# Kernel optimization log

Hardware: AMD Instinct MI355X
Metric: run time of the kernel (lower is better)

## Reference

```python
import jax, jax.numpy as jnp
import numpy as np

N_HEADS = 8
HEAD_C = 48
NC = N_HEADS * HEAD_C  # 384
N_GROUPS = 4
GC = NC // N_GROUPS  # 96
STRIDE = 2
EPS = 1e-5


def conv1x1(x, w, b):
    # x: (B,C,H,W), w: (O,C), b: (O,)
    return jnp.einsum('bchw,oc->bohw', x, w) + b[None, :, None, None]


def ref_points(Hk, Wk, dtype):
    ry = jnp.linspace(0.5, Hk - 0.5, Hk, dtype=dtype) / (Hk - 1.0) * 2.0 - 1.0
    rx = jnp.linspace(0.5, Wk - 0.5, Wk, dtype=dtype) / (Wk - 1.0) * 2.0 - 1.0
    return jnp.stack(jnp.meshgrid(ry, rx, indexing='ij'), axis=-1)  # (Hk,Wk,2) in (y,x)


def grid_sample_bilinear(img, grid):
    # img: (N,C,H,W); grid: (N,Hg,Wg,2) xy in [-1,1]; align_corners=True, zeros padding
    N, C, H, W = img.shape
    gx = (grid[..., 0] + 1.0) * 0.5 * (W - 1)
    gy = (grid[..., 1] + 1.0) * 0.5 * (H - 1)
    x0 = jnp.floor(gx); y0 = jnp.floor(gy)
    x1 = x0 + 1.0;      y1 = y0 + 1.0
    wx1 = gx - x0; wx0 = 1.0 - wx1
    wy1 = gy - y0; wy0 = 1.0 - wy1

    def gather(ix, iy):
        valid = (ix >= 0) & (ix <= W - 1) & (iy >= 0) & (iy <= H - 1)
        ixc = jnp.clip(ix, 0, W - 1).astype(jnp.int32)
        iyc = jnp.clip(iy, 0, H - 1).astype(jnp.int32)
        vals = jax.vmap(lambda im, yy, xx: im[:, yy, xx])(img, iyc, ixc)  # (N,C,Hg,Wg)
        return vals * valid[:, None].astype(img.dtype)

    v00 = gather(x0, y0); v01 = gather(x1, y0)
    v10 = gather(x0, y1); v11 = gather(x1, y1)
    return (v00 * (wx0 * wy0)[:, None] + v01 * (wx1 * wy0)[:, None]
            + v10 * (wx0 * wy1)[:, None] + v11 * (wx1 * wy1)[:, None])


def _forward(x, Wq, bq, Wk, bk, Wv, bv, Wo, bo,
             off_dw_w, off_dw_b, ln_g, ln_b, off_pw_w):
    B, C, H, W = x.shape
    q = conv1x1(x, Wq, bq)                               # (B,C,H,W)
    q_off = q.reshape(B * N_GROUPS, GC, H, W)
    # offset net: depthwise 3x3 stride-2 conv -> channel LN -> GELU -> 1x1 to 2 ch
    h = jax.lax.conv_general_dilated(
        q_off, off_dw_w, (STRIDE, STRIDE), ((1, 1), (1, 1)),
        dimension_numbers=('NCHW', 'OIHW', 'NCHW'), feature_group_count=GC)
    h = h + off_dw_b[None, :, None, None]
    mu = h.mean(axis=1, keepdims=True)
    var = ((h - mu) ** 2).mean(axis=1, keepdims=True)
    h = (h - mu) / jnp.sqrt(var + EPS) * ln_g[None, :, None, None] + ln_b[None, :, None, None]
    h = jax.nn.gelu(h, approximate=False)
    offset = jnp.einsum('bchw,oc->bohw', h, off_pw_w)    # (B*g, 2, Hk, Wk), ch0=y, ch1=x
    Hk, Wk_ = offset.shape[2], offset.shape[3]
    rng = jnp.array([1.0 / (Hk - 1.0), 1.0 / (Wk_ - 1.0)], x.dtype).reshape(1, 2, 1, 1)
    offset = jnp.tanh(offset) * rng                      # offset_range_factor = 1
    offset = offset.transpose(0, 2, 3, 1)                # (B*g, Hk, Wk, 2) yx
    ref = ref_points(Hk, Wk_, x.dtype)                   # (Hk, Wk, 2) yx
    pos = offset + ref[None]
    xs = grid_sample_bilinear(x.reshape(B * N_GROUPS, GC, H, W), pos[..., ::-1])
    n = Hk * Wk_
    xs = xs.reshape(B, C, 1, n)
    k = conv1x1(xs, Wk, bk).reshape(B * N_HEADS, HEAD_C, n)
    v = conv1x1(xs, Wv, bv).reshape(B * N_HEADS, HEAD_C, n)
    qh = q.reshape(B * N_HEADS, HEAD_C, H * W)
    attn = jnp.einsum('bcm,bcn->bmn', qh, k) * (HEAD_C ** -0.5)
    attn = jax.nn.softmax(attn, axis=2)
    out = jnp.einsum('bmn,bcn->bcm', attn, v).reshape(B, C, H, W)
    y = conv1x1(out, Wo, bo)
    ref_b = jnp.broadcast_to(ref[None, None], (B, N_GROUPS, Hk, Wk_, 2))
    return y, pos.reshape(B, N_GROUPS, Hk, Wk_, 2), ref_b


def setup_inputs() -> dict:
    key = jax.random.key(0)
    ks = jax.random.split(key, 12)
    s = 0.02
    return {
        'x': jax.random.normal(ks[0], (8, NC, 56, 56), jnp.float32),
        'Wq': jax.random.normal(ks[1], (NC, NC), jnp.float32) * s,
        'bq': jnp.zeros((NC,), jnp.float32),
        'Wk': jax.random.normal(ks[2], (NC, NC), jnp.float32) * s,
        'bk': jnp.zeros((NC,), jnp.float32),
        'Wv': jax.random.normal(ks[3], (NC, NC), jnp.float32) * s,
        'bv': jnp.zeros((NC,), jnp.float32),
        'Wo': jax.random.normal(ks[4], (NC, NC), jnp.float32) * s,
        'bo': jnp.zeros((NC,), jnp.float32),
        'off_dw_w': jax.random.normal(ks[5], (GC, 1, 3, 3), jnp.float32) * 0.1,
        'off_dw_b': jnp.zeros((GC,), jnp.float32),
        'ln_g': jnp.ones((GC,), jnp.float32),
        'ln_b': jnp.zeros((GC,), jnp.float32),
        'off_pw_w': jax.random.normal(ks[6], (2, GC), jnp.float32) * 0.1,
    }


def reference(x, Wq, bq, Wk, bk, Wv, bv, Wo, bo,
              off_dw_w, off_dw_b, ln_g, ln_b, off_pw_w):
    return _forward(x, Wq, bq, Wk, bk, Wv, bv, Wo, bo,
                    off_dw_w, off_dw_b, ln_g, ln_b, off_pw_w)
```

## Files before the change

### kernel.cpp

```cpp
#include <hip/hip_runtime.h>
#include <math.h>

constexpr int BATCH = 8;
constexpr int NC    = 384;
constexpr int H     = 56, W = 56, HW = 3136;
constexpr int NPTS  = 784;
constexpr int NG    = 4, GC = 96;
constexpr int NH    = 8, HC = 48;

typedef __attribute__((ext_vector_type(8))) short short8;
typedef __attribute__((ext_vector_type(4))) float f32x4;
typedef __attribute__((ext_vector_type(4))) unsigned short us4;

__device__ inline unsigned short f2bf(float f) {
    union { float f; unsigned u; } v; v.f = f;
    unsigned r = v.u + 0x7FFF + ((v.u >> 16) & 1);
    return (unsigned short)(r >> 16);
}
__device__ inline float bf2f(unsigned short u) {
    union { unsigned u; float f; } v; v.u = (unsigned)u << 16;
    return v.f;
}
__device__ inline float wred_sum(float v) {
    #pragma unroll
    for (int off = 32; off > 0; off >>= 1) v += __shfl_xor(v, off);
    return v;
}

__global__ __launch_bounds__(256) void transpose_cvt(
    const float* __restrict__ x, unsigned short* __restrict__ xT)
{
    __shared__ unsigned short Ls[64 * 68];
    int b = blockIdx.z, c0 = blockIdx.y * 64, hw0 = blockIdx.x * 64;
    const float* xb = x + ((size_t)b * NC + c0) * HW + hw0;
    int t = threadIdx.x;
    #pragma unroll
    for (int i = 0; i < 4; i++) {
        int u = t + i * 256;
        int cc = u >> 4, f4 = (u & 15) * 4;
        float4 v = *(const float4*)&xb[(size_t)cc * HW + f4];
        us4 p; p[0] = f2bf(v.x); p[1] = f2bf(v.y); p[2] = f2bf(v.z); p[3] = f2bf(v.w);
        *(us4*)&Ls[cc * 68 + f4] = p;
    }
    __syncthreads();
    unsigned short* xTb = xT + ((size_t)b * HW + hw0) * NC + c0;
    #pragma unroll
    for (int i = 0; i < 4; i++) {
        int u = t + i * 256;
        int hw = u >> 4, cg = (u & 15) * 4;
        us4 p;
        p[0] = Ls[(cg + 0) * 68 + hw];
        p[1] = Ls[(cg + 1) * 68 + hw];
        p[2] = Ls[(cg + 2) * 68 + hw];
        p[3] = Ls[(cg + 3) * 68 + hw];
        *(us4*)&xTb[(size_t)hw * NC + cg] = p;
    }
}

__global__ __launch_bounds__(256) void wcvt(
    const float* __restrict__ w0, const float* __restrict__ w1,
    const float* __restrict__ w2, const float* __restrict__ w3,
    unsigned short* __restrict__ o0, unsigned short* __restrict__ okv,
    unsigned short* __restrict__ o3)
{
    const float* src; unsigned short* dst;
    switch (blockIdx.y) {
        case 0: src = w0; dst = o0; break;
        case 1: src = w1; dst = okv; break;
        case 2: src = w2; dst = okv + NC * NC; break;
        default: src = w3; dst = o3; break;
    }
    int idx = (blockIdx.x * 256 + threadIdx.x) * 4;
    float4 v = *(const float4*)&src[idx];
    us4 p; p[0] = f2bf(v.x); p[1] = f2bf(v.y); p[2] = f2bf(v.z); p[3] = f2bf(v.w);
    *(us4*)&dst[idx] = p;
}

template<int MODE>
__global__ __launch_bounds__(256) void gemm_bf16(
    const unsigned short* __restrict__ A, const float* __restrict__ bias,
    const float* __restrict__ bias2, const unsigned short* __restrict__ BT,
    float* __restrict__ Cf, unsigned short* __restrict__ Cb,
    unsigned short* __restrict__ Cb2, int N)
{
    int b  = blockIdx.z;
    int n0 = blockIdx.x * 128;
    int m0 = blockIdx.y * 128;
    const unsigned short* BTb = BT + (size_t)b * N * NC;

    __shared__ unsigned short As[128 * 40];
    __shared__ unsigned short Bs[128 * 40];

    int t = threadIdx.x;
    int wave = t >> 6, lane = t & 63;
    int quad = lane >> 4, col = lane & 15;
    int wm = (wave >> 1) * 64, wn = (wave & 1) * 64;

    const short8 z8 = {0,0,0,0,0,0,0,0};
    f32x4 acc[4][4];
    #pragma unroll
    for (int i = 0; i < 4; i++)
        #pragma unroll
        for (int j = 0; j < 4; j++) acc[i][j] = (f32x4){0.f, 0.f, 0.f, 0.f};

    for (int k0 = 0; k0 < NC; k0 += 32) {
        #pragma unroll
        for (int i = 0; i < 2; i++) {
            int u = t + i * 256;
            int mm = u >> 2, kc = (u & 3) * 8;
            *(short8*)&As[mm * 40 + kc] =
                *(const short8*)&A[(size_t)(m0 + mm) * NC + k0 + kc];
        }
        #pragma unroll
        for (int i = 0; i < 2; i++) {
            int u = t + i * 256;
            int nn = u >> 2, kc = (u & 3) * 8;
            short8 val = z8;
            if (n0 + nn < N)
                val = *(const short8*)&BTb[(size_t)(n0 + nn) * NC + k0 + kc];
            *(short8*)&Bs[nn * 40 + kc] = val;
        }
        __syncthreads();

        short8 af[4], bf[4];
        #pragma unroll
        for (int mt = 0; mt < 4; mt++)
            af[mt] = *(const short8*)&As[(wm + mt * 16 + col) * 40 + quad * 8];
        #pragma unroll
        for (int nt = 0; nt < 4; nt++)
            bf[nt] = *(const short8*)&Bs[(wn + nt * 16 + col) * 40 + quad * 8];
        #pragma unroll
        for (int mt = 0; mt < 4; mt++)
            #pragma unroll
            for (int nt = 0; nt < 4; nt++)
                acc[mt][nt] = __builtin_amdgcn_mfma_f32_16x16x32_bf16(
                    af[mt], bf[nt], acc[mt][nt], 0, 0, 0);
        __syncthreads();
    }

    if constexpr (MODE == 0) {
        float* Cfb = Cf + (size_t)b * NC * N;
        #pragma unroll
        for (int mt = 0; mt < 4; mt++) {
            #pragma unroll
            for (int r = 0; r < 4; r++) {
                int m = m0 + wm + mt * 16 + quad * 4 + r;
                float bv = bias[m];
                #pragma unroll
                for (int nt = 0; nt < 4; nt++) {
                    int n = n0 + wn + nt * 16 + col;
                    if (n < N) Cfb[(size_t)m * N + n] = acc[mt][nt][r] + bv;
                }
            }
        }
    } else if constexpr (MODE == 2) {
        unsigned short* Kb = Cb + (size_t)b * N * NC;
        #pragma unroll
        for (int mt = 0; mt < 4; mt++) {
            int mb = m0 + wm + mt * 16 + quad * 4;
            float bv[4];
            #pragma unroll
            for (int r = 0; r < 4; r++) bv[r] = bias[mb + r];
            #pragma unroll
            for (int nt = 0; nt < 4; nt++) {
                int n = n0 + wn + nt * 16 + col;
                if (n < N) {
                    us4 p;
                    #pragma unroll
                    for (int r = 0; r < 4; r++) p[r] = f2bf(acc[mt][nt][r] + bv[r]);
                    *(us4*)&Kb[(size_t)n * NC + mb] = p;
                }
            }
        }
    } else {
        if (m0 < NC) {
            unsigned short* Kb = Cb + (size_t)b * N * NC;
            #pragma unroll
            for (int mt = 0; mt < 4; mt++) {
                int mb = m0 + wm + mt * 16 + quad * 4;
                float bv[4];
                #pragma unroll
                for (int r = 0; r < 4; r++) bv[r] = bias[mb + r];
                #pragma unroll
                for (int nt = 0; nt < 4; nt++) {
                    int n = n0 + wn + nt * 16 + col;
                    if (n < N) {
                        us4 p;
                        #pragma unroll
                        for (int r = 0; r < 4; r++) p[r] = f2bf(acc[mt][nt][r] + bv[r]);
                        *(us4*)&Kb[(size_t)n * NC + mb] = p;
                    }
                }
            }
        } else {
            unsigned short* Vb = Cb2 + (size_t)b * NC * N;
            #pragma unroll
            for (int mt = 0; mt < 4; mt++) {
                #pragma unroll
                for (int r = 0; r < 4; r++) {
                    int m = m0 - NC + wm + mt * 16 + quad * 4 + r;
                    float bv = bias2[m];
                    #pragma unroll
                    for (int nt = 0; nt < 4; nt++) {
                        int n = n0 + wn + nt * 16 + col;
                        if (n < N) Vb[(size_t)m * N + n] = f2bf(acc[mt][nt][r] + bv);
                    }
                }
            }
        }
    }
}

__global__ __launch_bounds__(256) void offset_kernel(
    const unsigned short* __restrict__ qT, const float* __restrict__ dww,
    const float* __restrict__ dwb, const float* __restrict__ lng,
    const float* __restrict__ lnb, const float* __restrict__ pww,
    float* __restrict__ pos_out,   float* __restrict__ ref_out)
{
    int wave = threadIdx.x >> 6, l = threadIdx.x & 63;
    int bg = blockIdx.y, b = bg >> 2, g = bg & 3;
    int s  = blockIdx.x * 4 + wave;
    int py = s / 28, px = s - py * 28;
    bool has2 = l < 32;
    int c0 = l, c1 = 64 + l;

    const unsigned short* qb = qT + (size_t)b * HW * NC + g * GC;

    float h0 = 0.f, h1 = 0.f;
    #pragma unroll
    for (int ky = 0; ky < 3; ky++) {
        int yy = py * 2 - 1 + ky;
        if (yy < 0 || yy >= H) continue;
        #pragma unroll
        for (int kx = 0; kx < 3; kx++) {
            int xx = px * 2 - 1 + kx;
            if (xx < 0 || xx >= W) continue;
            const unsigned short* row = qb + (size_t)(yy * W + xx) * NC;
            float w0 = dww[c0 * 9 + ky * 3 + kx];
            h0 = fmaf(bf2f(row[c0]), w0, h0);
            if (has2) {
                float w1 = dww[c1 * 9 + ky * 3 + kx];
                h1 = fmaf(bf2f(row[c1]), w1, h1);
            }
        }
    }
    h0 += dwb[c0];
    if (has2) h1 += dwb[c1];

    float mu = wred_sum(h0 + (has2 ? h1 : 0.f)) * (1.f / GC);
    float d0 = h0 - mu, d1 = h1 - mu;
    float var = wred_sum(d0 * d0 + (has2 ? d1 * d1 : 0.f)) * (1.f / GC);
    float rstd = rsqrtf(var + 1e-5f);

    float hn0 = d0 * rstd * lng[c0] + lnb[c0];
    float ge0 = 0.5f * hn0 * (1.f + erff(hn0 * 0.70710678118654752f));
    float ge1 = 0.f;
    if (has2) {
        float hn1 = d1 * rstd * lng[c1] + lnb[c1];
        ge1 = 0.5f * hn1 * (1.f + erff(hn1 * 0.70710678118654752f));
    }

    float offy = wred_sum(ge0 * pww[c0] + (has2 ? ge1 * pww[c1] : 0.f));
    float offx = wred_sum(ge0 * pww[GC + c0] + (has2 ? ge1 * pww[GC + c1] : 0.f));

    if (l == 0) {
        float ry = (2.f * py + 1.f) / 27.f - 1.f;
        float rx = (2.f * px + 1.f) / 27.f - 1.f;
        size_t idx = ((size_t)bg * NPTS + s) * 2;
        pos_out[idx]     = tanhf(offy) * (1.f / 27.f) + ry;
        pos_out[idx + 1] = tanhf(offx) * (1.f / 27.f) + rx;
        ref_out[idx]     = ry;
        ref_out[idx + 1] = rx;
    }
}

__global__ __launch_bounds__(256) void sample_kernel(
    const unsigned short* __restrict__ xT, const float* __restrict__ pos,
    unsigned short* __restrict__ xsT)
{
    int bg = blockIdx.y;
    int b  = bg >> 2, g = bg & 3;
    int s  = blockIdx.x * 8 + (threadIdx.x >> 5);
    int l  = threadIdx.x & 31;

    const float* pg = pos + ((size_t)bg * NPTS + s) * 2;
    float py = pg[0], px = pg[1];
    float gx = (px + 1.f) * 27.5f;
    float gy = (py + 1.f) * 27.5f;
    float x0f = floorf(gx), y0f = floorf(gy);
    int ix0 = (int)x0f, iy0 = (int)y0f;
    int ix1 = ix0 + 1,  iy1 = iy0 + 1;
    float wx1 = gx - x0f, wx0 = 1.f - wx1;
    float wy1 = gy - y0f, wy0 = 1.f - wy1;
    bool vx0 = (ix0 >= 0) && (ix0 < W);
    bool vx1 = (ix1 >= 0) && (ix1 < W);
    bool vy0 = (iy0 >= 0) && (iy0 < H);
    bool vy1 = (iy1 >= 0) && (iy1 < H);
    int cx0 = vx0 ? ix0 : 0, cx1 = vx1 ? ix1 : 0;
    int cy0 = vy0 ? iy0 : 0, cy1 = vy1 ? iy1 : 0;
    float w00 = (vx0 && vy0) ? wx0 * wy0 : 0.f;
    float w01 = (vx1 && vy0) ? wx1 * wy0 : 0.f;
    float w10 = (vx0 && vy1) ? wx0 * wy1 : 0.f;
    float w11 = (vx1 && vy1) ? wx1 * wy1 : 0.f;

    const unsigned short* xb = xT + (size_t)b * HW * NC + g * GC;
    const unsigned short* r00 = xb + (size_t)(cy0 * W + cx0) * NC;
    const unsigned short* r01 = xb + (size_t)(cy0 * W + cx1) * NC;
    const unsigned short* r10 = xb + (size_t)(cy1 * W + cx0) * NC;
    const unsigned short* r11 = xb + (size_t)(cy1 * W + cx1) * NC;
    unsigned short* orow = xsT + ((size_t)b * NPTS + s) * NC + g * GC;
    #pragma unroll
    for (int ci = 0; ci < 3; ci++) {
        int c = l + ci * 32;
        float val = bf2f(r00[c]) * w00 + bf2f(r01[c]) * w01
                  + bf2f(r10[c]) * w10 + bf2f(r11[c]) * w11;
        orow[c] = f2bf(val);
    }
}

#define KS_STRIDE 56
#define VS_STRIDE 136

__device__ inline short8 scale8(short8 v, float s) {
    short8 r;
    #pragma unroll
    for (int j = 0; j < 8; j++) {
        unsigned short b = (unsigned short)v[j];
        r[j] = (short)f2bf(bf2f(b) * s);
    }
    return r;
}

union pun8 { short8 s8; unsigned u[4]; };

__global__ __launch_bounds__(256) void attn_mfma(
    const unsigned short* __restrict__ qT, const unsigned short* __restrict__ kt,
    const unsigned short* __restrict__ vt, unsigned short* __restrict__ aoT)
{
    __shared__ __align__(16) unsigned short smem[128 * KS_STRIDE + 48 * VS_STRIDE];
    unsigned short* Ks = smem;
    unsigned short* Vs = Ks + 128 * KS_STRIDE;

    int t    = threadIdx.x;
    int wave = t >> 6, lane = t & 63;
    int quad = lane >> 4, col = lane & 15;

    int bh = blockIdx.y;
    int b  = bh >> 3, h = bh & 7;
    int m0 = blockIdx.x * 128;
    const unsigned short* KT = kt + (size_t)b * NPTS * NC + h * HC;
    const unsigned short* VT = vt + ((size_t)b * NC + h * HC) * NPTS;

    const float scale = 0.14433756729740643f * 1.4426950408889634f;
    const short8 z8 = {0,0,0,0,0,0,0,0};

    short ones_v = (col == 0) ? (short)0x3F80 : (short)0;
    short8 ones8 = {ones_v, ones_v, ones_v, ones_v, ones_v, ones_v, ones_v, ones_v};

    int gmq[2];
    short8 qb0[2], qb1[2];
    #pragma unroll
    for (int set = 0; set < 2; set++) {
        int gm = m0 + wave * 32 + set * 16 + col;
        gmq[set] = gm;
        int cg = gm < HW ? gm : HW - 1;
        const unsigned short* r0 = qT + ((size_t)b * HW + cg) * NC + h * HC;
        qb0[set] = scale8(*(const short8*)&r0[quad * 8], scale);
        qb1[set] = (quad < 2) ? scale8(*(const short8*)&r0[32 + quad * 8], scale) : z8;
    }

    f32x4 acc_l[2];
    f32x4 acc_o[2][3];
    #pragma unroll
    for (int set = 0; set < 2; set++) {
        acc_l[set] = (f32x4){0.f, 0.f, 0.f, 0.f};
        #pragma unroll
        for (int ct = 0; ct < 3; ct++) acc_o[set][ct] = (f32x4){0.f, 0.f, 0.f, 0.f};
    }

    int skey  = t >> 1;
    int spart = (t & 1) * 3;
    short8 kreg[3], vreg[3];

    {
        const unsigned short* krow = KT + (size_t)skey * NC + spart * 8;
        #pragma unroll
        for (int i = 0; i < 3; i++) kreg[i] = *(const short8*)(krow + i * 8);
        #pragma unroll
        for (int i = 0; i < 3; i++) {
            int li = t + i * 256;
            int chan = li >> 4, part = li & 15;
            vreg[i] = *(const short8*)&VT[(size_t)chan * NPTS + part * 8];
        }
    }

    for (int ci = 0; ci < 7; ci++) {
        int k0 = ci * 128;

        #pragma unroll
        for (int i = 0; i < 3; i++)
            *(short8*)&Ks[skey * KS_STRIDE + (spart + i) * 8] = kreg[i];
        #pragma unroll
        for (int i = 0; i < 3; i++) {
            int li = t + i * 256;
            int chan = li >> 4, part = li & 15;
            *(short8*)&Vs[chan * VS_STRIDE + part * 8] = vreg[i];
        }
        __syncthreads();

        if (ci < 6) {
            int nk0 = k0 + 128;
            bool kv = nk0 + skey < NPTS;
            const unsigned short* krow = KT + (size_t)(nk0 + skey) * NC + spart * 8;
            #pragma unroll
            for (int i = 0; i < 3; i++) kreg[i] = kv ? *(const short8*)(krow + i * 8) : z8;
            #pragma unroll
            for (int i = 0; i < 3; i++) {
                int li = t + i * 256;
                int chan = li >> 4, part = li & 15;
                vreg[i] = (nk0 + part * 8 < NPTS)
                    ? *(const short8*)&VT[(size_t)chan * NPTS + nk0 + part * 8] : z8;
            }
        }

        #pragma unroll
        for (int s2 = 0; s2 < 4; s2++) {
            if (k0 + s2 * 32 < NPTS) {
                unsigned pkd[2][2][2];
                #pragma unroll
                for (int jth = 0; jth < 2; jth++) {
                    int jt = s2 * 2 + jth;
                    int keyl = jt * 16 + col;
                    short8 kb0 = *(const short8*)&Ks[keyl * KS_STRIDE + quad * 8];
                    short8 kb1 = (quad < 2)
                        ? *(const short8*)&Ks[keyl * KS_STRIDE + 32 + quad * 8] : z8;
                    bool valid = (k0 + jt * 16) < NPTS;
                    #pragma unroll
                    for (int set = 0; set < 2; set++) {
                        f32x4 sa = {0.f, 0.f, 0.f, 0.f};
                        sa = __builtin_amdgcn_mfma_f32_16x16x32_bf16(kb0, qb0[set], sa, 0, 0, 0);
                        sa = __builtin_amdgcn_mfma_f32_16x16x32_bf16(kb1, qb1[set], sa, 0, 0, 0);
                        unsigned d0 = 0, d1 = 0;
                        if (valid) {
                            union { float f; unsigned u; } e0, e1, e2, e3;
                            e0.f = exp2f(sa[0]);
                            e1.f = exp2f(sa[1]);
                            e2.f = exp2f(sa[2]);
                            e3.f = exp2f(sa[3]);
                            d0 = __builtin_amdgcn_perm(e1.u, e0.u, 0x07060302u);
                            d1 = __builtin_amdgcn_perm(e3.u, e2.u, 0x07060302u);
                        }
                        pkd[set][jth][0] = d0;
                        pkd[set][jth][1] = d1;
                    }
                }
                short8 pb[2];
                #pragma unroll
                for (int set = 0; set < 2; set++) {
                    pun8 u;
                    u.u[0] = pkd[set][0][0]; u.u[1] = pkd[set][0][1];
                    u.u[2] = pkd[set][1][0]; u.u[3] = pkd[set][1][1];
                    pb[set] = u.s8;
                }
                #pragma unroll
                for (int ct = 0; ct < 3; ct++) {
                    const unsigned short* vrow =
                        &Vs[(ct * 16 + col) * VS_STRIDE + s2 * 32 + quad * 4];
                    pun8 uv;
                    uv.u[0] = *(const unsigned*)vrow;
                    uv.u[1] = *(const unsigned*)(vrow + 2);
                    uv.u[2] = *(const unsigned*)(vrow + 16);
                    uv.u[3] = *(const unsigned*)(vrow + 18);
                    short8 va = uv.s8;
                    #pragma unroll
                    for (int set = 0; set < 2; set++)
                        acc_o[set][ct] = __builtin_amdgcn_mfma_f32_16x16x32_bf16(
                            va, pb[set], acc_o[set][ct], 0, 0, 0);
                }
                #pragma unroll
                for (int set = 0; set < 2; set++)
                    acc_l[set] = __builtin_amdgcn_mfma_f32_16x16x32_bf16(
                        ones8, pb[set], acc_l[set], 0, 0, 0);
            }
        }
        __syncthreads();
    }

    #pragma unroll
    for (int set = 0; set < 2; set++) {
        float l = __shfl(acc_l[set][0], col);
        float inv = 1.f / l;
        int gm = gmq[set];
        if (gm < HW) {
            unsigned short* orow = aoT + ((size_t)b * HW + gm) * NC + h * HC;
            #pragma unroll
            for (int ct = 0; ct < 3; ct++) {
                us4 p;
                #pragma unroll
                for (int r = 0; r < 4; r++) p[r] = f2bf(acc_o[set][ct][r] * inv);
                *(us4*)&orow[ct * 16 + quad * 4] = p;
            }
        }
    }
}

extern "C" void kernel_launch(void* const* d_in, const int* in_sizes, int n_in,
                              void* d_out, int out_size, void* d_ws, size_t ws_size,
                              hipStream_t stream)
{
    const float* x   = (const float*)d_in[0];
    const float* Wq  = (const float*)d_in[1];
    const float* bq  = (const float*)d_in[2];
    const float* Wk  = (const float*)d_in[3];
    const float* bk  = (const float*)d_in[4];
    const float* Wv  = (const float*)d_in[5];
    const float* bv  = (const float*)d_in[6];
    const float* Wo  = (const float*)d_in[7];
    const float* bo  = (const float*)d_in[8];
    const float* dww = (const float*)d_in[9];
    const float* dwb = (const float*)d_in[10];
    const float* lng = (const float*)d_in[11];
    const float* lnb = (const float*)d_in[12];
    const float* pww = (const float*)d_in[13];

    float* out     = (float*)d_out;
    float* y_out   = out;
    float* pos_out = out + (size_t)BATCH * NC * HW;
    float* ref_out = pos_out + (size_t)BATCH * NG * NPTS * 2;

    const size_t NBIG = (size_t)BATCH * NC * HW;
    const size_t NSML = (size_t)BATCH * NC * NPTS;

    unsigned short* xT   = (unsigned short*)d_ws;
    unsigned short* qT   = xT   + NBIG;
    unsigned short* xsT  = qT   + NBIG;
    unsigned short* kt_w = xsT  + NSML;
    unsigned short* vt_w = kt_w + NSML;
    unsigned short* aoT  = vt_w + NSML;
    unsigned short* wqb  = aoT  + NBIG;
    unsigned short* wob  = wqb + NC * NC;
    unsigned short* wkv  = wob + NC * NC;

    transpose_cvt<<<dim3(49, 6, BATCH), 256, 0, stream>>>(x, xT);
    wcvt<<<dim3(144, 4), 256, 0, stream>>>(Wq, Wk, Wv, Wo, wqb, wkv, wob);
    gemm_bf16<2><<<dim3(25, 3, BATCH), 256, 0, stream>>>(
        wqb, bq, nullptr, xT, nullptr, qT, nullptr, HW);
    offset_kernel<<<dim3(196, BATCH * NG), 256, 0, stream>>>(
        qT, dww, dwb, lng, lnb, pww, pos_out, ref_out);
    sample_kernel<<<dim3(98, BATCH * NG), 256, 0, stream>>>(xT, pos_out, xsT);
    gemm_bf16<4><<<dim3(7, 6, BATCH), 256, 0, stream>>>(
        wkv, bk, bv, xsT, nullptr, kt_w, vt_w, NPTS);
    attn_mfma<<<dim3((HW + 127) / 128, BATCH * NH), 256, 0, stream>>>(
        qT, kt_w, vt_w, aoT);
    gemm_bf16<0><<<dim3(25, 3, BATCH), 256, 0, stream>>>(
        wob, bo, nullptr, aoT, y_out, nullptr, nullptr, HW);
}
```

Before: 294.9 us.

## Prefetch GEMM tiles into registers, vectorize sampling, pad K smem, use fast exp2

The GEMM kernel now loads the next K-slice from global memory into registers while the current slice is being computed, so load latency overlaps with the MFMA work. The bilinear sampling kernel uses 4-wide bf16 vector loads and stores on 24 lanes in place of scalar accesses on 32 lanes. The K shared-memory stride changes from 56 to 60, presumably to reduce LDS bank conflicts. exp2f is replaced by the hardware exp2 builtin. The register prefetch raises register pressure, and the builtin exp2 may handle denormals differently.

```diff
diff --git a/kernel.cpp b/kernel.cpp
--- a/kernel.cpp
+++ b/kernel.cpp
@@ -103,24 +103,31 @@
         #pragma unroll
         for (int j = 0; j < 4; j++) acc[i][j] = (f32x4){0.f, 0.f, 0.f, 0.f};
 
-    for (int k0 = 0; k0 < NC; k0 += 32) {
+    short8 areg[2], breg[2];
+    auto stage_load = [&](int k0) {
         #pragma unroll
         for (int i = 0; i < 2; i++) {
             int u = t + i * 256;
-            int mm = u >> 2, kc = (u & 3) * 8;
-            *(short8*)&As[mm * 40 + kc] =
-                *(const short8*)&A[(size_t)(m0 + mm) * NC + k0 + kc];
-        }
+            int mmi = u >> 2, kci = (u & 3) * 8;
+            areg[i] = *(const short8*)&A[(size_t)(m0 + mmi) * NC + k0 + kci];
+            short8 val = z8;
+            if (n0 + mmi < N)
+                val = *(const short8*)&BTb[(size_t)(n0 + mmi) * NC + k0 + kci];
+            breg[i] = val;
+        }
+    };
+
+    stage_load(0);
+    for (int k0 = 0; k0 < NC; k0 += 32) {
         #pragma unroll
         for (int i = 0; i < 2; i++) {
             int u = t + i * 256;
-            int nn = u >> 2, kc = (u & 3) * 8;
-            short8 val = z8;
-            if (n0 + nn < N)
-                val = *(const short8*)&BTb[(size_t)(n0 + nn) * NC + k0 + kc];
-            *(short8*)&Bs[nn * 40 + kc] = val;
+            int mmi = u >> 2, kci = (u & 3) * 8;
+            *(short8*)&As[mmi * 40 + kci] = areg[i];
+            *(short8*)&Bs[mmi * 40 + kci] = breg[i];
         }
         __syncthreads();
+        if (k0 + 32 < NC) stage_load(k0 + 32);
 
         short8 af[4], bf[4];
         #pragma unroll
@@ -303,22 +310,28 @@
     float w10 = (vx0 && vy1) ? wx0 * wy1 : 0.f;
     float w11 = (vx1 && vy1) ? wx1 * wy1 : 0.f;
 
-    const unsigned short* xb = xT + (size_t)b * HW * NC + g * GC;
-    const unsigned short* r00 = xb + (size_t)(cy0 * W + cx0) * NC;
-    const unsigned short* r01 = xb + (size_t)(cy0 * W + cx1) * NC;
-    const unsigned short* r10 = xb + (size_t)(cy1 * W + cx0) * NC;
-    const unsigned short* r11 = xb + (size_t)(cy1 * W + cx1) * NC;
-    unsigned short* orow = xsT + ((size_t)b * NPTS + s) * NC + g * GC;
-    #pragma unroll
-    for (int ci = 0; ci < 3; ci++) {
-        int c = l + ci * 32;
-        float val = bf2f(r00[c]) * w00 + bf2f(r01[c]) * w01
-                  + bf2f(r10[c]) * w10 + bf2f(r11[c]) * w11;
-        orow[c] = f2bf(val);
-    }
-}
-
-#define KS_STRIDE 56
+    if (l < 24) {
+        const unsigned short* xb = xT + (size_t)b * HW * NC + g * GC;
+        const unsigned short* r00 = xb + (size_t)(cy0 * W + cx0) * NC + l * 4;
+        const unsigned short* r01 = xb + (size_t)(cy0 * W + cx1) * NC + l * 4;
+        const unsigned short* r10 = xb + (size_t)(cy1 * W + cx0) * NC + l * 4;
+        const unsigned short* r11 = xb + (size_t)(cy1 * W + cx1) * NC + l * 4;
+        us4 a00 = *(const us4*)r00;
+        us4 a01 = *(const us4*)r01;
+        us4 a10 = *(const us4*)r10;
+        us4 a11 = *(const us4*)r11;
+        us4 o;
+        #pragma unroll
+        for (int j = 0; j < 4; j++) {
+            float val = bf2f(a00[j]) * w00 + bf2f(a01[j]) * w01
+                      + bf2f(a10[j]) * w10 + bf2f(a11[j]) * w11;
+            o[j] = f2bf(val);
+        }
+        *(us4*)&xsT[((size_t)b * NPTS + s) * NC + g * GC + l * 4] = o;
+    }
+}
+
+#define KS_STRIDE 60
 #define VS_STRIDE 136
 
 __device__ inline short8 scale8(short8 v, float s) {
@@ -443,10 +456,10 @@
                         unsigned d0 = 0, d1 = 0;
                         if (valid) {
                             union { float f; unsigned u; } e0, e1, e2, e3;
-                            e0.f = exp2f(sa[0]);
-                            e1.f = exp2f(sa[1]);
-                            e2.f = exp2f(sa[2]);
-                            e3.f = exp2f(sa[3]);
+                            e0.f = __builtin_amdgcn_exp2f(sa[0]);
+                            e1.f = __builtin_amdgcn_exp2f(sa[1]);
+                            e2.f = __builtin_amdgcn_exp2f(sa[2]);
+                            e3.f = __builtin_amdgcn_exp2f(sa[3]);
                             d0 = __builtin_amdgcn_perm(e1.u, e0.u, 0x07060302u);
                             d1 = __builtin_amdgcn_perm(e3.u, e2.u, 0x07060302u);
                         }
```

Measured after the change: 312.5 us. +6.0%, slower.
